# Kernel tuning notes

Measured on AMD Instinct MI355X. Metric: run time of the kernel, lower is better.

Reference implementation:

```python
import jax, jax.numpy as jnp
import numpy as np

D_MODEL = 1024
D_STATE = 64
D_CONV = 4
HEADDIM = 64
EXPAND = 2
NGROUPS = 1
D_INNER = EXPAND * D_MODEL            # 2048
NHEADS = D_INNER // HEADDIM           # 32
CONV_DIM = D_INNER + 2 * NGROUPS * D_STATE
D_IN_PROJ = 2 * D_INNER + 2 * NGROUPS * D_STATE + NHEADS
FFN_DIM = 4096
B_SZ = 2
SEQ = 2048


def layernorm(x, w, b, eps=1e-5):
    m = jnp.mean(x, axis=-1, keepdims=True)
    v = jnp.var(x, axis=-1, keepdims=True)
    return (x - m) * jax.lax.rsqrt(v + eps) * w + b


def silu(x):
    return x * jax.nn.sigmoid(x)


def causal_dwconv(x, w, b):
    # x: [B, L, C], w: [C, K] depthwise, b: [C]; causal (left) padding
    xc = jnp.transpose(x, (0, 2, 1))                       # [B, C, L]
    xc = jnp.pad(xc, ((0, 0), (0, 0), (D_CONV - 1, 0)))
    k = w[:, None, :]                                      # [C, 1, K]
    y = jax.lax.conv_general_dilated(
        xc, k, window_strides=(1,), padding='VALID',
        dimension_numbers=('NCH', 'OIH', 'NCH'),
        feature_group_count=CONV_DIM)
    return jnp.transpose(y, (0, 2, 1)) + b                 # [B, L, C]


def mamba2(x, in_proj_w, conv_w, conv_b, dt_bias, A_log, D_param, norm_w, out_proj_w):
    Bsz, L, _ = x.shape
    zxbcdt = x @ in_proj_w.T                               # [B, L, D_IN_PROJ]
    z, xBC, dt = jnp.split(zxbcdt, [D_INNER, D_INNER + CONV_DIM], axis=-1)
    dt = jax.nn.softplus(dt + dt_bias)                     # [B, L, H]
    xBC = silu(causal_dwconv(xBC, conv_w, conv_b))
    xs, Bm, Cm = jnp.split(xBC, [D_INNER, D_INNER + NGROUPS * D_STATE], axis=-1)
    xs = xs.reshape(Bsz, L, NHEADS, HEADDIM)
    Bm = Bm.reshape(Bsz, L, NGROUPS, D_STATE)
    Cm = Cm.reshape(Bsz, L, NGROUPS, D_STATE)
    hpg = NHEADS // NGROUPS
    Bh = jnp.repeat(Bm, hpg, axis=2)                       # [B, L, H, N]
    Ch = jnp.repeat(Cm, hpg, axis=2)                       # [B, L, H, N]
    A = -jnp.exp(A_log)                                    # [H]
    dA = jnp.exp(dt * A)                                   # [B, L, H]

    # time-major for scan
    def step(h, inp):
        dA_t, dt_t, x_t, B_t, C_t = inp                    # [B,H], [B,H], [B,H,P], [B,H,N], [B,H,N]
        h = h * dA_t[:, :, None, None] + (dt_t[:, :, None, None] * x_t[..., None]) * B_t[:, :, None, :]
        y_t = jnp.einsum('bhpn,bhn->bhp', h, C_t)
        return h, y_t

    h0 = jnp.zeros((Bsz, NHEADS, HEADDIM, D_STATE), dtype=x.dtype)
    xs_tm = (jnp.moveaxis(dA, 1, 0), jnp.moveaxis(dt, 1, 0),
             jnp.moveaxis(xs, 1, 0), jnp.moveaxis(Bh, 1, 0), jnp.moveaxis(Ch, 1, 0))
    _, ys = jax.lax.scan(step, h0, xs_tm)                  # [L, B, H, P]
    y = jnp.moveaxis(ys, 0, 1) + D_param[None, None, :, None] * xs
    y = y.reshape(Bsz, L, D_INNER)
    # gated RMSNorm: RMSNorm(y * silu(z)) * weight
    y = y * silu(z)
    y = y * jax.lax.rsqrt(jnp.mean(jnp.square(y), axis=-1, keepdims=True) + 1e-5) * norm_w
    return y @ out_proj_w.T                                # [B, L, D_MODEL]


def setup_inputs() -> dict:
    key = jax.random.key(0)
    ks = jax.random.split(key, 12)
    s = 0.02
    inp = {
        'x': jax.random.normal(ks[0], (B_SZ, SEQ, D_MODEL), dtype=jnp.float32),
        'ln0_w': jnp.ones((D_MODEL,), jnp.float32), 'ln0_b': jnp.zeros((D_MODEL,), jnp.float32),
        'ln1_w': jnp.ones((D_MODEL,), jnp.float32), 'ln1_b': jnp.zeros((D_MODEL,), jnp.float32),
        'ln2_w': jnp.ones((D_MODEL,), jnp.float32), 'ln2_b': jnp.zeros((D_MODEL,), jnp.float32),
        'in_proj_w': jax.random.normal(ks[1], (D_IN_PROJ, D_MODEL), jnp.float32) * s,
        'conv_w': jax.random.normal(ks[2], (CONV_DIM, D_CONV), jnp.float32) * 0.2,
        'conv_b': jnp.zeros((CONV_DIM,), jnp.float32),
        'dt_bias': jax.random.uniform(ks[3], (NHEADS,), jnp.float32, -4.0, -1.0),
        'A_log': jnp.log(jnp.arange(1, NHEADS + 1, dtype=jnp.float32)),
        'D_param': jnp.ones((NHEADS,), jnp.float32),
        'norm_w': jnp.ones((D_INNER,), jnp.float32),
        'out_proj_w': jax.random.normal(ks[4], (D_MODEL, D_INNER), jnp.float32) * s,
        'ffn_w1': jax.random.normal(ks[5], (FFN_DIM, D_MODEL), jnp.float32) * s,
        'ffn_b1': jnp.zeros((FFN_DIM,), jnp.float32),
        'ffn_w2': jax.random.normal(ks[6], (D_MODEL, FFN_DIM), jnp.float32) * s,
        'ffn_b2': jnp.zeros((D_MODEL,), jnp.float32),
    }
    return inp


def reference(x, ln0_w, ln0_b, ln1_w, ln1_b, ln2_w, ln2_b, in_proj_w, conv_w, conv_b,
              dt_bias, A_log, D_param, norm_w, out_proj_w, ffn_w1, ffn_b1, ffn_w2, ffn_b2):
    x = layernorm(x, ln0_w, ln0_b)                                  # ln0 (layer_id==0)
    m = mamba2(layernorm(x, ln1_w, ln1_b), in_proj_w, conv_w, conv_b,
               dt_bias, A_log, D_param, norm_w, out_proj_w)
    x = x + m                                                        # dropout is identity in eval
    h = layernorm(x, ln2_w, ln2_b)
    h = jax.nn.gelu(h @ ffn_w1.T + ffn_b1, approximate=False) @ ffn_w2.T + ffn_b2
    return x + h
```

## Files before the change

kernel.cpp:

```cpp
#include <hip/hip_runtime.h>
#include <hip/hip_bf16.h>
#include <math.h>

typedef __hip_bfloat16 bf16;
typedef __bf16 bhalf;
typedef bhalf bhalf8 __attribute__((ext_vector_type(8)));
typedef float f32x4 __attribute__((ext_vector_type(4)));
typedef unsigned short u16;
typedef u16 u16x4 __attribute__((ext_vector_type(4)));

#define D_MODEL   1024
#define D_STATE   64
#define HEADDIM   64
#define D_INNER   2048
#define NHEADS    32
#define CONV_DIM  2176
#define D_IN_PROJ 4256
#define FFN_DIM   4096
#define BSZ       2
#define SEQ       2048
#define NROWS     (BSZ*SEQ)
#define TC        64
#define NCH       (SEQ/TC)

#define AS1 __attribute__((address_space(1)))
#define AS3 __attribute__((address_space(3)))
__device__ __forceinline__ void load_lds16(const void* g, void* l) {
  __builtin_amdgcn_global_load_lds((AS1 void*)g, (AS3 void*)l, 16, 0, 0);
}

__global__ __launch_bounds__(64)
void detect_kernel(const unsigned short* __restrict__ x, int* __restrict__ flagp)
{
  int bad = 0;
  for (int i = threadIdx.x; i < 4096; i += 64) {
    unsigned u = ((unsigned)x[i]) << 16;
    float v = __uint_as_float(u);
    if (!(fabsf(v) <= 1e6f)) bad = 1;
  }
  unsigned long long any = __ballot(bad);
  if (threadIdx.x == 0) *flagp = (any != 0ULL) ? 1 : 0;
}

#define NT 19
struct CvtArgs {
  const void* src[NT];
  void*       dst[NT];
  int ccum[NT + 1];
  int nel[NT];
};

__global__ __launch_bounds__(256)
void cvt_kernel(CvtArgs a, const int* __restrict__ flagp)
{
  int c = blockIdx.x;
  int ti = 0;
  while (c >= a.ccum[ti + 1]) ti++;
  int base = (c - a.ccum[ti]) * 2048;
  int n = a.nel[ti];
  if (*flagp) {
    const float* s = (const float*)a.src[ti];
    bf16* d = (bf16*)a.dst[ti];
    for (int i = threadIdx.x; i < 2048; i += 256) {
      int j = base + i;
      if (j < n) d[j] = __float2bfloat16(s[j]);
    }
  } else {
    const unsigned short* s = (const unsigned short*)a.src[ti];
    unsigned short* d = (unsigned short*)a.dst[ti];
    for (int i = threadIdx.x; i < 2048; i += 256) {
      int j = base + i;
      if (j < n) d[j] = s[j];
    }
  }
}

template<int EPI>
__global__ __launch_bounds__(256, 2)
void gemm_bt(const bf16* __restrict__ A, const bf16* __restrict__ W,
             int M, int N, int K,
             bf16* __restrict__ outB,
             const bf16* __restrict__ bias)
{
  __shared__ __align__(16) bhalf sA[128 * 32];
  __shared__ __align__(16) bhalf sW[128 * 32];
  const int t    = threadIdx.x;
  const int n0   = blockIdx.x * 128;
  const int m0   = blockIdx.y * 128;
  const int w    = t >> 6;
  const int lane = t & 63;
  const int wm   = (w >> 1) * 64;
  const int wn   = (w & 1) * 64;
  const int lr   = lane & 15;
  const int lq   = lane >> 4;
  const int srow = t >> 2;
  const int scol = (t & 3) * 8;

  f32x4 acc[4][4];
  #pragma unroll
  for (int i = 0; i < 4; i++)
    #pragma unroll
    for (int j = 0; j < 4; j++)
      acc[i][j] = (f32x4){0.f, 0.f, 0.f, 0.f};

  for (int k0 = 0; k0 < K; k0 += 32) {
    #pragma unroll
    for (int hh = 0; hh < 2; hh++) {
      int row = hh * 64 + srow;
      load_lds16(A + (size_t)(m0 + row) * K + k0 + scol, sA + hh * 2048 + t * 8);
      int wr = n0 + row; wr = wr < N ? wr : N - 1;
      load_lds16(W + (size_t)wr * K + k0 + scol, sW + hh * 2048 + t * 8);
    }
    __syncthreads();
    bhalf8 af[4], bfr[4];
    #pragma unroll
    for (int i = 0; i < 4; i++)
      af[i] = *(const bhalf8*)(sA + (wm + i * 16 + lr) * 32 + lq * 8);
    #pragma unroll
    for (int j = 0; j < 4; j++)
      bfr[j] = *(const bhalf8*)(sW + (wn + j * 16 + lr) * 32 + lq * 8);
    #pragma unroll
    for (int i = 0; i < 4; i++)
      #pragma unroll
      for (int j = 0; j < 4; j++)
        acc[i][j] = __builtin_amdgcn_mfma_f32_16x16x32_bf16(af[i], bfr[j], acc[i][j], 0, 0, 0);
    __syncthreads();
  }

  #pragma unroll
  for (int i = 0; i < 4; i++) {
    #pragma unroll
    for (int j = 0; j < 4; j++) {
      #pragma unroll
      for (int r = 0; r < 4; r++) {
        int m = m0 + wm + i * 16 + lq * 4 + r;
        int n = n0 + wn + j * 16 + lr;
        if (n < N) {
          float v = acc[i][j][r];
          size_t idx = (size_t)m * N + n;
          if (EPI == 0) {
            outB[idx] = __float2bfloat16(v);
          } else {
            v += __bfloat162float(bias[n]);
            outB[idx] = __float2bfloat16(0.5f * v * (1.0f + erff(v * 0.70710678118654752f)));
          }
        }
      }
    }
  }
}

struct SkParts { float* p0; float* p1; float* p2; float* p3; };

__global__ __launch_bounds__(256, 2)
void gemm_sk(const bf16* __restrict__ A, const bf16* __restrict__ W,
             int M, int N, int K, int ks, SkParts parts)
{
  __shared__ __align__(16) bhalf sA[128 * 32];
  __shared__ __align__(16) bhalf sW[128 * 32];
  const int t    = threadIdx.x;
  const int n0   = blockIdx.x * 128;
  const int m0   = blockIdx.y * 128;
  const int z    = blockIdx.z;
  const int w    = t >> 6;
  const int lane = t & 63;
  const int wm   = (w >> 1) * 64;
  const int wn   = (w & 1) * 64;
  const int lr   = lane & 15;
  const int lq   = lane >> 4;
  const int srow = t >> 2;
  const int scol = (t & 3) * 8;

  f32x4 acc[4][4];
  #pragma unroll
  for (int i = 0; i < 4; i++)
    #pragma unroll
    for (int j = 0; j < 4; j++)
      acc[i][j] = (f32x4){0.f, 0.f, 0.f, 0.f};

  const int kend = z * ks + ks;
  for (int k0 = z * ks; k0 < kend; k0 += 32) {
    #pragma unroll
    for (int hh = 0; hh < 2; hh++) {
      int row = hh * 64 + srow;
      load_lds16(A + (size_t)(m0 + row) * K + k0 + scol, sA + hh * 2048 + t * 8);
      load_lds16(W + (size_t)(n0 + row) * K + k0 + scol, sW + hh * 2048 + t * 8);
    }
    __syncthreads();
    bhalf8 af[4], bfr[4];
    #pragma unroll
    for (int i = 0; i < 4; i++)
      af[i] = *(const bhalf8*)(sA + (wm + i * 16 + lr) * 32 + lq * 8);
    #pragma unroll
    for (int j = 0; j < 4; j++)
      bfr[j] = *(const bhalf8*)(sW + (wn + j * 16 + lr) * 32 + lq * 8);
    #pragma unroll
    for (int i = 0; i < 4; i++)
      #pragma unroll
      for (int j = 0; j < 4; j++)
        acc[i][j] = __builtin_amdgcn_mfma_f32_16x16x32_bf16(af[i], bfr[j], acc[i][j], 0, 0, 0);
    __syncthreads();
  }

  float* out = (z == 0) ? parts.p0 : (z == 1) ? parts.p1 : (z == 2) ? parts.p2 : parts.p3;
  #pragma unroll
  for (int i = 0; i < 4; i++)
    #pragma unroll
    for (int j = 0; j < 4; j++)
      #pragma unroll
      for (int r = 0; r < 4; r++) {
        int m = m0 + wm + i * 16 + lq * 4 + r;
        int n = n0 + wn + j * 16 + lr;
        out[(size_t)m * N + n] = acc[i][j][r];
      }
}

__global__ __launch_bounds__(256)
void reduce_out_kernel(const float* __restrict__ p0, const float* __restrict__ p1,
                       const bf16* __restrict__ resB, float* __restrict__ out)
{
  int i = blockIdx.x * 256 + threadIdx.x;
  f32x4 a = ((const f32x4*)p0)[i];
  f32x4 b = ((const f32x4*)p1)[i];
  u16x4 r = ((const u16x4*)resB)[i];
  f32x4 o;
  #pragma unroll
  for (int j = 0; j < 4; j++)
    o[j] = a[j] + b[j] + __uint_as_float(((unsigned)r[j]) << 16);
  ((f32x4*)out)[i] = o;
}

__global__ __launch_bounds__(256)
void reduce_ffn_kernel(const float* __restrict__ p0, const float* __restrict__ p1,
                       const float* __restrict__ p2, const float* __restrict__ p3,
                       const bf16* __restrict__ bias, const float* __restrict__ resF,
                       void* __restrict__ outp, const int* __restrict__ flagp)
{
  int i = blockIdx.x * 256 + threadIdx.x;
  int n4 = i & (D_MODEL / 4 - 1);
  f32x4 v0 = ((const f32x4*)p0)[i];
  f32x4 v1 = ((const f32x4*)p1)[i];
  f32x4 v2 = ((const f32x4*)p2)[i];
  f32x4 v3 = ((const f32x4*)p3)[i];
  f32x4 rf = ((const f32x4*)resF)[i];
  u16x4 bb = ((const u16x4*)bias)[n4];
  f32x4 o;
  #pragma unroll
  for (int j = 0; j < 4; j++)
    o[j] = ((v0[j] + v1[j]) + (v2[j] + v3[j])) + rf[j] +
           __uint_as_float(((unsigned)bb[j]) << 16);
  if (*flagp) {
    ((f32x4*)outp)[i] = o;
  } else {
    bf16* ob = (bf16*)outp;
    #pragma unroll
    for (int j = 0; j < 4; j++) ob[i * 4 + j] = __float2bfloat16(o[j]);
  }
}

__global__ __launch_bounds__(256)
void ln01_kernel(const bf16* __restrict__ x,
                 const bf16* __restrict__ w0, const bf16* __restrict__ b0,
                 const bf16* __restrict__ w1, const bf16* __restrict__ b1,
                 bf16* __restrict__ x0o, bf16* __restrict__ x1o)
{
  int row = blockIdx.x, t = threadIdx.x;
  const bf16* xr = x + (size_t)row * D_MODEL;
  __shared__ float rs[4], rq[4];
  float v[4], s = 0.f, ss = 0.f;
  #pragma unroll
  for (int i = 0; i < 4; i++) {
    v[i] = __bfloat162float(xr[t + 256 * i]);
    s += v[i]; ss += v[i] * v[i];
  }
  #pragma unroll
  for (int o = 32; o; o >>= 1) { s += __shfl_down(s, o); ss += __shfl_down(ss, o); }
  if ((t & 63) == 0) { rs[t >> 6] = s; rq[t >> 6] = ss; }
  __syncthreads();
  float S = rs[0] + rs[1] + rs[2] + rs[3];
  float Q = rq[0] + rq[1] + rq[2] + rq[3];
  float mean = S * (1.f / D_MODEL);
  float rstd = rsqrtf(Q * (1.f / D_MODEL) - mean * mean + 1e-5f);
  float u[4]; s = 0.f; ss = 0.f;
  #pragma unroll
  for (int i = 0; i < 4; i++) {
    int c = t + 256 * i;
    u[i] = (v[i] - mean) * rstd * __bfloat162float(w0[c]) + __bfloat162float(b0[c]);
    s += u[i]; ss += u[i] * u[i];
    x0o[(size_t)row * D_MODEL + c] = __float2bfloat16(u[i]);
  }
  __syncthreads();
  #pragma unroll
  for (int o = 32; o; o >>= 1) { s += __shfl_down(s, o); ss += __shfl_down(ss, o); }
  if ((t & 63) == 0) { rs[t >> 6] = s; rq[t >> 6] = ss; }
  __syncthreads();
  S = rs[0] + rs[1] + rs[2] + rs[3];
  Q = rq[0] + rq[1] + rq[2] + rq[3];
  mean = S * (1.f / D_MODEL);
  rstd = rsqrtf(Q * (1.f / D_MODEL) - mean * mean + 1e-5f);
  #pragma unroll
  for (int i = 0; i < 4; i++) {
    int c = t + 256 * i;
    x1o[(size_t)row * D_MODEL + c] =
        __float2bfloat16((u[i] - mean) * rstd * __bfloat162float(w1[c]) + __bfloat162float(b1[c]));
  }
}

__global__ __launch_bounds__(256)
void conv_silu_kernel(const bf16* __restrict__ zxb, const bf16* __restrict__ cw,
                      const bf16* __restrict__ cb, float* __restrict__ xact)
{
  int c = blockIdx.x * 256 + threadIdx.x;
  int row = blockIdx.y;
  if (c >= CONV_DIM) return;
  int l = row & (SEQ - 1);
  float acc = __bfloat162float(cb[c]);
  #pragma unroll
  for (int k = 0; k < 4; k++) {
    int lt = l - 3 + k;
    if (lt >= 0)
      acc += __bfloat162float(zxb[(size_t)(row - 3 + k) * D_IN_PROJ + D_INNER + c]) *
             __bfloat162float(cw[c * 4 + k]);
  }
  xact[(size_t)row * CONV_DIM + c] = acc / (1.f + expf(-acc));
}

__global__ __launch_bounds__(256)
void dt_kernel(const bf16* __restrict__ zxb, const bf16* __restrict__ dt_bias,
               const bf16* __restrict__ A_log, float* __restrict__ dts,
               float* __restrict__ ldab)
{
  int i = blockIdx.x * 256 + threadIdx.x;
  int row = i >> 5, h = i & 31;
  float v = __bfloat162float(zxb[(size_t)row * D_IN_PROJ + (D_INNER + CONV_DIM) + h]) +
            __bfloat162float(dt_bias[h]);
  float sp = (v > 20.f) ? v : log1pf(expf(v));
  dts[i] = sp;
  ldab[i] = -sp * expf(__bfloat162float(A_log[h]));
}

__global__ __launch_bounds__(256)
void scan_state_kernel(const float* __restrict__ xact, const float* __restrict__ dts,
                       const float* __restrict__ ldab, bf16* __restrict__ Sbuf,
                       float* __restrict__ acb)
{
  __shared__ __align__(16) bf16 wBT[64][72];
  __shared__ __align__(16) bf16 XT[64][72];
  __shared__ float lsS[64], dtS[64];
  const int bid = blockIdx.x;
  const int bh = bid & 63, c = bid >> 6;
  const int b = bh >> 5, h = bh & 31;
  const int t0 = c * TC;
  const int tid = threadIdx.x;
  const int w = tid >> 6, lane = tid & 63;
  const int lr = lane & 15, lq = lane >> 4;

  if (w == 0) {
    float v = ldab[(size_t)(b * SEQ + t0 + lane) * NHEADS + h];
    #pragma unroll
    for (int o = 1; o < 64; o <<= 1) {
      float up = __shfl_up(v, o);
      if (lane >= o) v += up;
    }
    lsS[lane] = v;
    dtS[lane] = dts[(size_t)(b * SEQ + t0 + lane) * NHEADS + h];
  }
  __syncthreads();
  const float lsT = lsS[63];
  {
    int nn = tid & 63, u0 = (tid >> 6) * 16;
    for (int i = 0; i < 16; i++) {
      int u = u0 + i;
      const float* rowp = xact + (size_t)(b * SEQ + t0 + u) * CONV_DIM;
      float wgt = dtS[u] * __expf(lsT - lsS[u]);
      wBT[nn][u] = __float2bfloat16(rowp[D_INNER + nn] * wgt);
      XT[nn][u]  = __float2bfloat16(rowp[h * 64 + nn]);
    }
  }
  __syncthreads();

  bhalf8 af0 = *(const bhalf8*)&wBT[16 * w + lr][lq * 8];
  bhalf8 af1 = *(const bhalf8*)&wBT[16 * w + lr][32 + lq * 8];
  bf16* sb = Sbuf + ((size_t)bh * NCH + c) * 4096;
  #pragma unroll
  for (int jt = 0; jt < 4; jt++) {
    bhalf8 xf0 = *(const bhalf8*)&XT[16 * jt + lr][lq * 8];
    bhalf8 xf1 = *(const bhalf8*)&XT[16 * jt + lr][32 + lq * 8];
    f32x4 acc = (f32x4){0.f, 0.f, 0.f, 0.f};
    acc = __builtin_amdgcn_mfma_f32_16x16x32_bf16(af0, xf0, acc, 0, 0, 0);
    acc = __builtin_amdgcn_mfma_f32_16x16x32_bf16(af1, xf1, acc, 0, 0, 0);
    #pragma unroll
    for (int r = 0; r < 4; r++) {
      int n = 16 * w + lq * 4 + r;
      int p = 16 * jt + lr;
      sb[p * 64 + n] = __float2bfloat16(acc[r]);
    }
  }
  if (tid == 0) acb[bh * NCH + c] = __expf(lsT);
}

__global__ __launch_bounds__(256)
void state_prop_kernel(bf16* __restrict__ Sbuf, const float* __restrict__ acb)
{
  const int bh = blockIdx.x >> 2, q = blockIdx.x & 3;
  const int t = threadIdx.x;
  bf16* sp = Sbuf + (size_t)bh * NCH * 4096 + q * 1024 + t;
  const float* ap = acb + bh * NCH;
  float h0 = 0.f, h1 = 0.f, h2 = 0.f, h3 = 0.f;
  for (int c = 0; c < NCH; c++) {
    bf16* pc = sp + (size_t)c * 4096;
    float s0 = __bfloat162float(pc[0]);
    float s1 = __bfloat162float(pc[256]);
    float s2 = __bfloat162float(pc[512]);
    float s3 = __bfloat162float(pc[768]);
    float a = ap[c];
    pc[0]   = __float2bfloat16(h0);
    pc[256] = __float2bfloat16(h1);
    pc[512] = __float2bfloat16(h2);
    pc[768] = __float2bfloat16(h3);
    h0 = fmaf(h0, a, s0); h1 = fmaf(h1, a, s1);
    h2 = fmaf(h2, a, s2); h3 = fmaf(h3, a, s3);
  }
}

__global__ __launch_bounds__(256)
void scan_y_kernel(const float* __restrict__ xact, const float* __restrict__ dts,
                   const float* __restrict__ ldab, const bf16* __restrict__ Sbuf,
                   bf16* __restrict__ yfull)
{
  __shared__ __align__(16) bf16 Cs[64][72];
  __shared__ __align__(16) bf16 Bs[64][72];
  __shared__ __align__(16) bf16 XT[64][72];
  __shared__ __align__(16) bf16 HT[64][72];
  __shared__ __align__(16) bf16 Ms[64][72];
  __shared__ float lsS[64], dtS[64];
  const int bid = blockIdx.x;
  const int bh = bid & 63, c = bid >> 6;
  const int b = bh >> 5, h = bh & 31;
  const int t0 = c * TC;
  const int tid = threadIdx.x;
  const int w = tid >> 6, lane = tid & 63;
  const int lr = lane & 15, lq = lane >> 4;

  if (w == 0) {
    float v = ldab[(size_t)(b * SEQ + t0 + lane) * NHEADS + h];
    #pragma unroll
    for (int o = 1; o < 64; o <<= 1) {
      float up = __shfl_up(v, o);
      if (lane >= o) v += up;
    }
    lsS[lane] = v;
    dtS[lane] = dts[(size_t)(b * SEQ + t0 + lane) * NHEADS + h];
  }
  {
    int nn = tid & 63, u0 = (tid >> 6) * 16;
    for (int i = 0; i < 16; i++) {
      int u = u0 + i;
      const float* rowp = xact + (size_t)(b * SEQ + t0 + u) * CONV_DIM;
      Bs[u][nn] = __float2bfloat16(rowp[D_INNER + nn]);
      Cs[u][nn] = __float2bfloat16(rowp[D_INNER + 64 + nn]);
      XT[nn][u] = __float2bfloat16(rowp[h * 64 + nn]);
    }
    const bf16* sb = Sbuf + ((size_t)bh * NCH + c) * 4096;
    for (int i = 0; i < 16; i++) {
      int e = tid + 256 * i;
      HT[e >> 6][e & 63] = sb[e];
    }
  }
  __syncthreads();

  bhalf8 cf0 = *(const bhalf8*)&Cs[16 * w + lr][lq * 8];
  bhalf8 cf1 = *(const bhalf8*)&Cs[16 * w + lr][32 + lq * 8];
  f32x4 accH[4];
  #pragma unroll
  for (int jt = 0; jt < 4; jt++) {
    bhalf8 bf0 = *(const bhalf8*)&Bs[16 * jt + lr][lq * 8];
    bhalf8 bf1 = *(const bhalf8*)&Bs[16 * jt + lr][32 + lq * 8];
    f32x4 g = (f32x4){0.f, 0.f, 0.f, 0.f};
    g = __builtin_amdgcn_mfma_f32_16x16x32_bf16(cf0, bf0, g, 0, 0, 0);
    g = __builtin_amdgcn_mfma_f32_16x16x32_bf16(cf1, bf1, g, 0, 0, 0);
    bhalf8 hf0 = *(const bhalf8*)&HT[16 * jt + lr][lq * 8];
    bhalf8 hf1 = *(const bhalf8*)&HT[16 * jt + lr][32 + lq * 8];
    f32x4 ah = (f32x4){0.f, 0.f, 0.f, 0.f};
    ah = __builtin_amdgcn_mfma_f32_16x16x32_bf16(cf0, hf0, ah, 0, 0, 0);
    ah = __builtin_amdgcn_mfma_f32_16x16x32_bf16(cf1, hf1, ah, 0, 0, 0);
    accH[jt] = ah;
    #pragma unroll
    for (int r = 0; r < 4; r++) {
      int t = 16 * w + lq * 4 + r;
      int u = 16 * jt + lr;
      float m = 0.f;
      if (u <= t) m = g[r] * __expf(lsS[t] - lsS[u]) * dtS[u];
      Ms[t][u] = __float2bfloat16(m);
    }
  }
  __syncthreads();

  bhalf8 mf0 = *(const bhalf8*)&Ms[16 * w + lr][lq * 8];
  bhalf8 mf1 = *(const bhalf8*)&Ms[16 * w + lr][32 + lq * 8];
  #pragma unroll
  for (int jt = 0; jt < 4; jt++) {
    bhalf8 xf0 = *(const bhalf8*)&XT[16 * jt + lr][lq * 8];
    bhalf8 xf1 = *(const bhalf8*)&XT[16 * jt + lr][32 + lq * 8];
    f32x4 acc = (f32x4){0.f, 0.f, 0.f, 0.f};
    acc = __builtin_amdgcn_mfma_f32_16x16x32_bf16(mf0, xf0, acc, 0, 0, 0);
    acc = __builtin_amdgcn_mfma_f32_16x16x32_bf16(mf1, xf1, acc, 0, 0, 0);
    #pragma unroll
    for (int r = 0; r < 4; r++) {
      int t = 16 * w + lq * 4 + r;
      int p = 16 * jt + lr;
      float y = acc[r] + __expf(lsS[t]) * accH[jt][r];
      yfull[(size_t)(b * SEQ + t0 + t) * D_INNER + h * 64 + p] = __float2bfloat16(y);
    }
  }
}

__global__ __launch_bounds__(256)
void gate_rms_kernel(const bf16* __restrict__ yfull, const float* __restrict__ xact,
                     const bf16* __restrict__ zxb, const bf16* __restrict__ Dp,
                     const bf16* __restrict__ nw, bf16* __restrict__ yn)
{
  int row = blockIdx.x, t = threadIdx.x;
  __shared__ float rq[4];
  float yv[8]; float ss = 0.f;
  #pragma unroll
  for (int i = 0; i < 8; i++) {
    int c = t + 256 * i;
    float y = __bfloat162float(yfull[(size_t)row * D_INNER + c]) +
              __bfloat162float(Dp[c >> 6]) * xact[(size_t)row * CONV_DIM + c];
    float z = __bfloat162float(zxb[(size_t)row * D_IN_PROJ + c]);
    yv[i] = y * (z / (1.f + expf(-z)));
    ss += yv[i] * yv[i];
  }
  #pragma unroll
  for (int o = 32; o; o >>= 1) ss += __shfl_down(ss, o);
  if ((t & 63) == 0) rq[t >> 6] = ss;
  __syncthreads();
  float tot = rq[0] + rq[1] + rq[2] + rq[3];
  float rr = rsqrtf(tot * (1.f / D_INNER) + 1e-5f);
  #pragma unroll
  for (int i = 0; i < 8; i++) {
    int c = t + 256 * i;
    yn[(size_t)row * D_INNER + c] =
        __float2bfloat16(yv[i] * rr * __bfloat162float(nw[c]));
  }
}

__global__ __launch_bounds__(256)
void ln2_kernel(const float* __restrict__ xin, const bf16* __restrict__ w,
                const bf16* __restrict__ b, bf16* __restrict__ out)
{
  int row = blockIdx.x, t = threadIdx.x;
  const float* xr = xin + (size_t)row * D_MODEL;
  __shared__ float rs[4], rq[4];
  float v[4], s = 0.f, ss = 0.f;
  #pragma unroll
  for (int i = 0; i < 4; i++) {
    v[i] = xr[t + 256 * i];
    s += v[i]; ss += v[i] * v[i];
  }
  #pragma unroll
  for (int o = 32; o; o >>= 1) { s += __shfl_down(s, o); ss += __shfl_down(ss, o); }
  if ((t & 63) == 0) { rs[t >> 6] = s; rq[t >> 6] = ss; }
  __syncthreads();
  float S = rs[0] + rs[1] + rs[2] + rs[3];
  float Q = rq[0] + rq[1] + rq[2] + rq[3];
  float mean = S * (1.f / D_MODEL);
  float rstd = rsqrtf(Q * (1.f / D_MODEL) - mean * mean + 1e-5f);
  #pragma unroll
  for (int i = 0; i < 4; i++) {
    int c = t + 256 * i;
    out[(size_t)row * D_MODEL + c] =
        __float2bfloat16((v[i] - mean) * rstd * __bfloat162float(w[c]) + __bfloat162float(b[c]));
  }
}

extern "C" void kernel_launch(void* const* d_in, const int* in_sizes, int n_in,
                              void* d_out, int out_size, void* d_ws, size_t ws_size,
                              hipStream_t stream)
{
  char* ws = (char*)d_ws;
  bf16*  xcvt  = (bf16*) (ws + 0);
  bf16*  x1b   = (bf16*) (ws + 8388608);
  bf16*  Sbuf  = (bf16*) (ws + 0);
  bf16*  ynb   = (bf16*) (ws + 0);
  float* pf0   = (float*)(ws + 0);
  bf16*  wproj = (bf16*) (ws + 16777216);
  float* acb   = (float*)(ws + 16777216);
  float* dtsb  = (float*)(ws + 16785408);
  float* ldab  = (float*)(ws + 17309696);
  float* pf1   = (float*)(ws + 16777216);
  bf16*  wout  = (bf16*) (ws + 25493504);
  bf16*  w1c   = (bf16*) (ws + 29687808);
  bf16*  w2c   = (bf16*) (ws + 38076416);
  bf16*  ln0w  = (bf16*) (ws + 46465024);
  bf16*  ln0b  = (bf16*) (ws + 46467072);
  bf16*  ln1w  = (bf16*) (ws + 46469120);
  bf16*  ln1b  = (bf16*) (ws + 46471168);
  bf16*  ln2w  = (bf16*) (ws + 46473216);
  bf16*  ln2b  = (bf16*) (ws + 46475264);
  bf16*  convw = (bf16*) (ws + 46477312);
  bf16*  convb = (bf16*) (ws + 46494720);
  bf16*  dtb   = (bf16*) (ws + 46499072);
  bf16*  alog  = (bf16*) (ws + 46499136);
  bf16*  Dp    = (bf16*) (ws + 46499200);
  bf16*  normw = (bf16*) (ws + 46499264);
  bf16*  b1c   = (bf16*) (ws + 46503360);
  bf16*  b2c   = (bf16*) (ws + 46511552);
  int*   flag  = (int*)  (ws + 46513600);
  bf16*  x0b   = (bf16*) (ws + 46514176);
  bf16*  zxb   = (bf16*) (ws + 54902784);
  float* x2f   = (float*)(ws + 54902784);
  float* pf3   = (float*)(ws + 71680000);
  float* xact  = (float*)(ws + 89767936);
  float* pout0 = (float*)(ws + 89767936);
  float* pout1 = (float*)(ws + 106545152);
  bf16*  gbuf  = (bf16*) (ws + 89767936);
  bf16*  yfull = (bf16*) (ws + 125419520);
  bf16*  hln   = (bf16*) (ws + 125419520);
  float* pf2   = (float*)(ws + 125419520);

  detect_kernel<<<1, 64, 0, stream>>>((const unsigned short*)d_in[0], flag);

  CvtArgs ca;
  void* dsts[NT] = { xcvt, ln0w, ln0b, ln1w, ln1b, ln2w, ln2b, wproj, convw, convb,
                     dtb, alog, Dp, normw, wout, w1c, b1c, w2c, b2c };
  int cc = 0;
  ca.ccum[0] = 0;
  for (int i = 0; i < NT; i++) {
    ca.src[i] = d_in[i];
    ca.dst[i] = dsts[i];
    ca.nel[i] = in_sizes[i];
    cc += (in_sizes[i] + 2047) / 2048;
    ca.ccum[i + 1] = cc;
  }
  cvt_kernel<<<cc, 256, 0, stream>>>(ca, flag);

  ln01_kernel<<<NROWS, 256, 0, stream>>>(xcvt, ln0w, ln0b, ln1w, ln1b, x0b, x1b);

  gemm_bt<0><<<dim3(34, 32), 256, 0, stream>>>(x1b, wproj, NROWS, D_IN_PROJ, D_MODEL,
                                               zxb, nullptr);

  conv_silu_kernel<<<dim3(9, NROWS), 256, 0, stream>>>(zxb, convw, convb, xact);
  dt_kernel<<<(NROWS * NHEADS) / 256, 256, 0, stream>>>(zxb, dtb, alog, dtsb, ldab);

  scan_state_kernel<<<NCH * 64, 256, 0, stream>>>(xact, dtsb, ldab, Sbuf, acb);
  state_prop_kernel<<<64 * 4, 256, 0, stream>>>(Sbuf, acb);
  scan_y_kernel<<<NCH * 64, 256, 0, stream>>>(xact, dtsb, ldab, Sbuf, yfull);

  gate_rms_kernel<<<NROWS, 256, 0, stream>>>(yfull, xact, zxb, Dp, normw, ynb);

  SkParts po = { pout0, pout1, pout0, pout0 };
  gemm_sk<<<dim3(8, 32, 2), 256, 0, stream>>>(ynb, wout, NROWS, D_MODEL, D_INNER, 1024, po);
  reduce_out_kernel<<<(NROWS * D_MODEL) / 1024, 256, 0, stream>>>(pout0, pout1, x0b, x2f);

  ln2_kernel<<<NROWS, 256, 0, stream>>>(x2f, ln2w, ln2b, hln);

  gemm_bt<2><<<dim3(32, 32), 256, 0, stream>>>(hln, w1c, NROWS, FFN_DIM, D_MODEL,
                                               gbuf, b1c);

  SkParts pfp = { pf0, pf1, pf2, pf3 };
  gemm_sk<<<dim3(8, 32, 4), 256, 0, stream>>>(gbuf, w2c, NROWS, D_MODEL, FFN_DIM, 1024, pfp);
  reduce_ffn_kernel<<<(NROWS * D_MODEL) / 1024, 256, 0, stream>>>(pf0, pf1, pf2, pf3,
                                                                  b2c, x2f, d_out, flag);
}
```

Baseline: 510.9 us.

## Deepen GEMM K-tile to 64 with XOR-swizzled LDS; store conv activations in bf16

Both GEMM kernels now stage a 64-wide K slice per iteration instead of 32. The LDS layout uses an XOR swizzle on 16-byte chunks to avoid bank conflicts on fragment reads, and there are half as many barrier pairs per unit of work. Separately, the conv+SiLU output buffer changes from fp32 to bf16, which halves its write and read traffic in the scan and gate kernels. The costs are doubled LDS per block, which may limit the two blocks per CU, and slightly lower precision on the skip-connection term.

```diff
diff --git a/kernel.cpp b/kernel.cpp
--- a/kernel.cpp
+++ b/kernel.cpp
@@ -82,8 +82,8 @@
              bf16* __restrict__ outB,
              const bf16* __restrict__ bias)
 {
-  __shared__ __align__(16) bhalf sA[128 * 32];
-  __shared__ __align__(16) bhalf sW[128 * 32];
+  __shared__ __align__(16) bhalf sA[128 * 64];
+  __shared__ __align__(16) bhalf sW[128 * 64];
   const int t    = threadIdx.x;
   const int n0   = blockIdx.x * 128;
   const int m0   = blockIdx.y * 128;
@@ -93,8 +93,6 @@
   const int wn   = (w & 1) * 64;
   const int lr   = lane & 15;
   const int lq   = lane >> 4;
-  const int srow = t >> 2;
-  const int scol = (t & 3) * 8;
 
   f32x4 acc[4][4];
   #pragma unroll
@@ -103,27 +101,38 @@
     for (int j = 0; j < 4; j++)
       acc[i][j] = (f32x4){0.f, 0.f, 0.f, 0.f};
 
-  for (int k0 = 0; k0 < K; k0 += 32) {
-    #pragma unroll
-    for (int hh = 0; hh < 2; hh++) {
-      int row = hh * 64 + srow;
-      load_lds16(A + (size_t)(m0 + row) * K + k0 + scol, sA + hh * 2048 + t * 8);
-      int wr = n0 + row; wr = wr < N ? wr : N - 1;
-      load_lds16(W + (size_t)wr * K + k0 + scol, sW + hh * 2048 + t * 8);
+  for (int k0 = 0; k0 < K; k0 += 64) {
+    #pragma unroll
+    for (int j = 0; j < 4; j++) {
+      int s  = t + 256 * j;
+      int r  = s >> 3;
+      int cs = (s & 7) ^ (r & 7);
+      load_lds16(A + (size_t)(m0 + r) * K + k0 + cs * 8, sA + s * 8);
+      int wr = n0 + r; wr = wr < N ? wr : N - 1;
+      load_lds16(W + (size_t)wr * K + k0 + cs * 8, sW + s * 8);
     }
     __syncthreads();
-    bhalf8 af[4], bfr[4];
-    #pragma unroll
-    for (int i = 0; i < 4; i++)
-      af[i] = *(const bhalf8*)(sA + (wm + i * 16 + lr) * 32 + lq * 8);
-    #pragma unroll
-    for (int j = 0; j < 4; j++)
-      bfr[j] = *(const bhalf8*)(sW + (wn + j * 16 + lr) * 32 + lq * 8);
-    #pragma unroll
-    for (int i = 0; i < 4; i++)
-      #pragma unroll
-      for (int j = 0; j < 4; j++)
-        acc[i][j] = __builtin_amdgcn_mfma_f32_16x16x32_bf16(af[i], bfr[j], acc[i][j], 0, 0, 0);
+    #pragma unroll
+    for (int kk = 0; kk < 2; kk++) {
+      bhalf8 af[4], bfr[4];
+      #pragma unroll
+      for (int i = 0; i < 4; i++) {
+        int r = wm + i * 16 + lr;
+        int c = (kk * 4 + lq) ^ (r & 7);
+        af[i] = *(const bhalf8*)(sA + r * 64 + c * 8);
+      }
+      #pragma unroll
+      for (int j = 0; j < 4; j++) {
+        int r = wn + j * 16 + lr;
+        int c = (kk * 4 + lq) ^ (r & 7);
+        bfr[j] = *(const bhalf8*)(sW + r * 64 + c * 8);
+      }
+      #pragma unroll
+      for (int i = 0; i < 4; i++)
+        #pragma unroll
+        for (int j = 0; j < 4; j++)
+          acc[i][j] = __builtin_amdgcn_mfma_f32_16x16x32_bf16(af[i], bfr[j], acc[i][j], 0, 0, 0);
+    }
     __syncthreads();
   }
 
@@ -156,8 +165,8 @@
 void gemm_sk(const bf16* __restrict__ A, const bf16* __restrict__ W,
              int M, int N, int K, int ks, SkParts parts)
 {
-  __shared__ __align__(16) bhalf sA[128 * 32];
-  __shared__ __align__(16) bhalf sW[128 * 32];
+  __shared__ __align__(16) bhalf sA[128 * 64];
+  __shared__ __align__(16) bhalf sW[128 * 64];
   const int t    = threadIdx.x;
   const int n0   = blockIdx.x * 128;
   const int m0   = blockIdx.y * 128;
@@ -168,8 +177,6 @@
   const int wn   = (w & 1) * 64;
   const int lr   = lane & 15;
   const int lq   = lane >> 4;
-  const int srow = t >> 2;
-  const int scol = (t & 3) * 8;
 
   f32x4 acc[4][4];
   #pragma unroll
@@ -179,26 +186,37 @@
       acc[i][j] = (f32x4){0.f, 0.f, 0.f, 0.f};
 
   const int kend = z * ks + ks;
-  for (int k0 = z * ks; k0 < kend; k0 += 32) {
-    #pragma unroll
-    for (int hh = 0; hh < 2; hh++) {
-      int row = hh * 64 + srow;
-      load_lds16(A + (size_t)(m0 + row) * K + k0 + scol, sA + hh * 2048 + t * 8);
-      load_lds16(W + (size_t)(n0 + row) * K + k0 + scol, sW + hh * 2048 + t * 8);
+  for (int k0 = z * ks; k0 < kend; k0 += 64) {
+    #pragma unroll
+    for (int j = 0; j < 4; j++) {
+      int s  = t + 256 * j;
+      int r  = s >> 3;
+      int cs = (s & 7) ^ (r & 7);
+      load_lds16(A + (size_t)(m0 + r) * K + k0 + cs * 8, sA + s * 8);
+      load_lds16(W + (size_t)(n0 + r) * K + k0 + cs * 8, sW + s * 8);
     }
     __syncthreads();
-    bhalf8 af[4], bfr[4];
-    #pragma unroll
-    for (int i = 0; i < 4; i++)
-      af[i] = *(const bhalf8*)(sA + (wm + i * 16 + lr) * 32 + lq * 8);
-    #pragma unroll
-    for (int j = 0; j < 4; j++)
-      bfr[j] = *(const bhalf8*)(sW + (wn + j * 16 + lr) * 32 + lq * 8);
-    #pragma unroll
-    for (int i = 0; i < 4; i++)
-      #pragma unroll
-      for (int j = 0; j < 4; j++)
-        acc[i][j] = __builtin_amdgcn_mfma_f32_16x16x32_bf16(af[i], bfr[j], acc[i][j], 0, 0, 0);
+    #pragma unroll
+    for (int kk = 0; kk < 2; kk++) {
+      bhalf8 af[4], bfr[4];
+      #pragma unroll
+      for (int i = 0; i < 4; i++) {
+        int r = wm + i * 16 + lr;
+        int c = (kk * 4 + lq) ^ (r & 7);
+        af[i] = *(const bhalf8*)(sA + r * 64 + c * 8);
+      }
+      #pragma unroll
+      for (int j = 0; j < 4; j++) {
+        int r = wn + j * 16 + lr;
+        int c = (kk * 4 + lq) ^ (r & 7);
+        bfr[j] = *(const bhalf8*)(sW + r * 64 + c * 8);
+      }
+      #pragma unroll
+      for (int i = 0; i < 4; i++)
+        #pragma unroll
+        for (int j = 0; j < 4; j++)
+          acc[i][j] = __builtin_amdgcn_mfma_f32_16x16x32_bf16(af[i], bfr[j], acc[i][j], 0, 0, 0);
+    }
     __syncthreads();
   }
 
@@ -308,7 +326,7 @@
 
 __global__ __launch_bounds__(256)
 void conv_silu_kernel(const bf16* __restrict__ zxb, const bf16* __restrict__ cw,
-                      const bf16* __restrict__ cb, float* __restrict__ xact)
+                      const bf16* __restrict__ cb, bf16* __restrict__ xact)
 {
   int c = blockIdx.x * 256 + threadIdx.x;
   int row = blockIdx.y;
@@ -322,7 +340,7 @@
       acc += __bfloat162float(zxb[(size_t)(row - 3 + k) * D_IN_PROJ + D_INNER + c]) *
              __bfloat162float(cw[c * 4 + k]);
   }
-  xact[(size_t)row * CONV_DIM + c] = acc / (1.f + expf(-acc));
+  xact[(size_t)row * CONV_DIM + c] = __float2bfloat16(acc / (1.f + expf(-acc)));
 }
 
 __global__ __launch_bounds__(256)
@@ -340,7 +358,7 @@
 }
 
 __global__ __launch_bounds__(256)
-void scan_state_kernel(const float* __restrict__ xact, const float* __restrict__ dts,
+void scan_state_kernel(const bf16* __restrict__ xact, const float* __restrict__ dts,
                        const float* __restrict__ ldab, bf16* __restrict__ Sbuf,
                        float* __restrict__ acb)
 {
@@ -371,10 +389,10 @@
     int nn = tid & 63, u0 = (tid >> 6) * 16;
     for (int i = 0; i < 16; i++) {
       int u = u0 + i;
-      const float* rowp = xact + (size_t)(b * SEQ + t0 + u) * CONV_DIM;
+      const bf16* rowp = xact + (size_t)(b * SEQ + t0 + u) * CONV_DIM;
       float wgt = dtS[u] * __expf(lsT - lsS[u]);
-      wBT[nn][u] = __float2bfloat16(rowp[D_INNER + nn] * wgt);
-      XT[nn][u]  = __float2bfloat16(rowp[h * 64 + nn]);
+      wBT[nn][u] = __float2bfloat16(__bfloat162float(rowp[D_INNER + nn]) * wgt);
+      XT[nn][u]  = rowp[h * 64 + nn];
     }
   }
   __syncthreads();
@@ -424,7 +442,7 @@
 }
 
 __global__ __launch_bounds__(256)
-void scan_y_kernel(const float* __restrict__ xact, const float* __restrict__ dts,
+void scan_y_kernel(const bf16* __restrict__ xact, const float* __restrict__ dts,
                    const float* __restrict__ ldab, const bf16* __restrict__ Sbuf,
                    bf16* __restrict__ yfull)
 {
@@ -456,10 +474,10 @@
     int nn = tid & 63, u0 = (tid >> 6) * 16;
     for (int i = 0; i < 16; i++) {
       int u = u0 + i;
-      const float* rowp = xact + (size_t)(b * SEQ + t0 + u) * CONV_DIM;
-      Bs[u][nn] = __float2bfloat16(rowp[D_INNER + nn]);
-      Cs[u][nn] = __float2bfloat16(rowp[D_INNER + 64 + nn]);
-      XT[nn][u] = __float2bfloat16(rowp[h * 64 + nn]);
+      const bf16* rowp = xact + (size_t)(b * SEQ + t0 + u) * CONV_DIM;
+      Bs[u][nn] = rowp[D_INNER + nn];
+      Cs[u][nn] = rowp[D_INNER + 64 + nn];
+      XT[nn][u] = rowp[h * 64 + nn];
     }
     const bf16* sb = Sbuf + ((size_t)bh * NCH + c) * 4096;
     for (int i = 0; i < 16; i++) {
@@ -516,7 +534,7 @@
 }
 
 __global__ __launch_bounds__(256)
-void gate_rms_kernel(const bf16* __restrict__ yfull, const float* __restrict__ xact,
+void gate_rms_kernel(const bf16* __restrict__ yfull, const bf16* __restrict__ xact,
                      const bf16* __restrict__ zxb, const bf16* __restrict__ Dp,
                      const bf16* __restrict__ nw, bf16* __restrict__ yn)
 {
@@ -527,7 +545,8 @@
   for (int i = 0; i < 8; i++) {
     int c = t + 256 * i;
     float y = __bfloat162float(yfull[(size_t)row * D_INNER + c]) +
-              __bfloat162float(Dp[c >> 6]) * xact[(size_t)row * CONV_DIM + c];
+              __bfloat162float(Dp[c >> 6]) *
+              __bfloat162float(xact[(size_t)row * CONV_DIM + c]);
     float z = __bfloat162float(zxb[(size_t)row * D_IN_PROJ + c]);
     yv[i] = y * (z / (1.f + expf(-z)));
     ss += yv[i] * yv[i];
@@ -612,7 +631,7 @@
   bf16*  zxb   = (bf16*) (ws + 54902784);
   float* x2f   = (float*)(ws + 54902784);
   float* pf3   = (float*)(ws + 71680000);
-  float* xact  = (float*)(ws + 89767936);
+  bf16*  xact  = (bf16*) (ws + 89767936);
   float* pout0 = (float*)(ws + 89767936);
   float* pout1 = (float*)(ws + 106545152);
   bf16*  gbuf  = (bf16*) (ws + 89767936);
```

Result: faster. 481.0 us (-5.9%).
